# Kernel tuning notes

Measured on AMD Instinct MI355X. Metric: run time of the kernel, lower is better.

The kernel has to match this reference:

```python
import jax, jax.numpy as jnp
import numpy as np

VOCAB_SIZE = 32000
HIDDEN_DIM = 1024
NUM_BUF_ACTIONS = 128
BATCH = 64
SEQ_LEN = 512


def setup_inputs() -> dict:
    key = jax.random.key(0)
    ks = jax.random.split(key, 8)
    H = HIDDEN_DIM
    x = jax.random.randint(ks[0], (BATCH, SEQ_LEN), 0, VOCAB_SIZE, dtype=jnp.int32)
    true_actions = jax.random.randint(ks[1], (BATCH, SEQ_LEN), 0, NUM_BUF_ACTIONS, dtype=jnp.int32)
    true_states = jax.random.randint(ks[2], (BATCH, SEQ_LEN), 0, NUM_BUF_ACTIONS, dtype=jnp.int32)
    use_forcing = 0
    # Learned params: embedding table, LSTM input/recurrent kernels (gate order i,f,g,o), dense head
    embed = jax.random.normal(ks[3], (VOCAB_SIZE, H), dtype=jnp.float32) * 0.02
    Wi = jax.random.normal(ks[4], (H, 4 * H), dtype=jnp.float32) * (1.0 / np.sqrt(H))
    Wh = jax.random.normal(ks[5], (H, 4 * H), dtype=jnp.float32) * (1.0 / np.sqrt(H))
    bh = jnp.zeros((4 * H,), dtype=jnp.float32)
    Wo = jax.random.normal(ks[6], (H, NUM_BUF_ACTIONS), dtype=jnp.float32) * (1.0 / np.sqrt(H))
    bo = jnp.zeros((NUM_BUF_ACTIONS,), dtype=jnp.float32)
    return {"embed": embed, "Wi": Wi, "Wh": Wh, "bh": bh, "Wo": Wo, "bo": bo,
            "x": x, "true_actions": true_actions, "true_states": true_states,
            "use_forcing": use_forcing}


def _lstm_forward(embed, Wi, Wh, bh, Wo, bo, x):
    B, S = x.shape
    H = embed.shape[1]
    x_emb = embed[x]                                    # [B,S,H]
    # Precompute input-side gate projections for all timesteps (one big GEMM)
    gx = jnp.einsum('bsh,hg->sbg', x_emb, Wi)           # [S,B,4H]
    c0 = jnp.zeros((B, H), dtype=x_emb.dtype)
    h0 = jnp.zeros((B, H), dtype=x_emb.dtype)

    def step(carry, gx_t):
        c, h = carry
        gates = gx_t + h @ Wh + bh                      # [B,4H]
        i, f, g, o = jnp.split(gates, 4, axis=-1)
        i = jax.nn.sigmoid(i)
        f = jax.nn.sigmoid(f)
        g = jnp.tanh(g)
        o = jax.nn.sigmoid(o)
        c = f * c + i * g
        h = o * jnp.tanh(c)
        return (c, h), h

    _, hs = jax.lax.scan(step, (c0, h0), gx)            # hs: [S,B,H]
    hs = jnp.transpose(hs, (1, 0, 2))                   # [B,S,H]
    logits_buf = hs @ Wo + bo                           # [B,S,A]
    dummy = jnp.zeros((B, S, 1), dtype=logits_buf.dtype)
    return dummy, logits_buf, dummy


def reference(embed, Wi, Wh, bh, Wo, bo, x, true_actions, true_states, use_forcing):
    # true_actions/true_states/use_forcing are unused in the original forward
    return _lstm_forward(embed, Wi, Wh, bh, Wo, bo, x)
```

## Files before the change

### kernel.cpp

```cpp
#include <hip/hip_runtime.h>
#include <hip/hip_bf16.h>

typedef __attribute__((ext_vector_type(8))) short short8;
typedef __attribute__((ext_vector_type(4))) float float4v;
typedef __attribute__((ext_vector_type(4))) unsigned int uint4v;
typedef unsigned short ushort_t;
typedef unsigned int uint_t;

#define BB 64
#define SS 512
#define HH 1024
#define AA 128
#define NWG 256

#define XSW_BYTES   67108864ULL
#define WSW_BYTES   16777216ULL
#define HALL_BYTES  67239936ULL
#define XSW_OFF     0ULL
#define WSW_OFF     (XSW_OFF + XSW_BYTES)
#define HALL_OFF    (WSW_OFF + WSW_BYTES)
#define FLAGS_OFF   (HALL_OFF + HALL_BYTES)

__device__ __forceinline__ ushort_t f2bf(float f) {
    union { float f; uint_t u; } v; v.f = f;
    uint_t u = v.u;
    return (ushort_t)((u + 0x7fffu + ((u >> 16) & 1u)) >> 16);
}

__device__ __forceinline__ float fast_sigmoid(float x) {
    return __builtin_amdgcn_rcpf(1.0f + __expf(-x));
}
__device__ __forceinline__ float fast_tanh(float x) {
    return 1.0f - 2.0f * __builtin_amdgcn_rcpf(1.0f + __expf(2.0f * x));
}

__global__ void k_init(uint_t* __restrict__ flags, ushort_t* __restrict__ hall,
                       float* __restrict__ out) {
    int i = blockIdx.x * 256 + threadIdx.x;
    if (i < NWG) flags[i] = 0u;
    ((uint_t*)hall)[i] = 0u;
    out[i] = 0.0f;
    out[32768 + (size_t)BB * SS * AA + i] = 0.0f;
}

__global__ void k_prep_x(const float* __restrict__ embed, const int* __restrict__ x,
                         ushort_t* __restrict__ xsw) {
    int t = blockIdx.x * 256 + threadIdx.x;
    int lane = t & 63;
    int rg   = (t >> 6) & 3;
    int kk   = (t >> 8) & 31;
    int s    = t >> 13;
    int b  = rg * 16 + (lane & 15);
    int k0 = kk * 32 + (lane >> 4) * 8;
    int tok = x[b * SS + s];
    const float* src = embed + (size_t)tok * HH + k0;
    float4v v0 = *(const float4v*)src;
    float4v v1 = *(const float4v*)(src + 4);
    uint_t p0 = (uint_t)f2bf(v0[0]) | ((uint_t)f2bf(v0[1]) << 16);
    uint_t p1 = (uint_t)f2bf(v0[2]) | ((uint_t)f2bf(v0[3]) << 16);
    uint_t p2 = (uint_t)f2bf(v1[0]) | ((uint_t)f2bf(v1[1]) << 16);
    uint_t p3 = (uint_t)f2bf(v1[2]) | ((uint_t)f2bf(v1[3]) << 16);
    uint4v pk = {p0, p1, p2, p3};
    ((uint4v*)xsw)[t] = pk;
}

__global__ void k_prep_w(const float* __restrict__ Wi, const float* __restrict__ Wh,
                         ushort_t* __restrict__ wsw) {
    int t = blockIdx.x * 256 + threadIdx.x;
    int u = t & 1023;
    int q = (t >> 10) & 3;
    int k = t >> 12;
    float v = (k < 1024) ? Wi[(size_t)k * 4096 + q * 1024 + u]
                         : Wh[(size_t)(k - 1024) * 4096 + q * 1024 + u];
    int g = u >> 2, du = u & 3;
    int c = du * 4 + q;
    int kk = k >> 5, quad = (k >> 3) & 3, j = k & 7;
    int lane = quad * 16 + c;
    wsw[(((size_t)g * 64 + kk) * 64 + lane) * 8 + j] = f2bf(v);
}

__global__ void __launch_bounds__(256)
k_lstm(const ushort_t* __restrict__ xsw, const ushort_t* __restrict__ wsw,
       ushort_t* hall, const float* __restrict__ bh, uint_t* flags) {
    __shared__ ushort_t wlds[64 * 64 * 8];
    const int g    = blockIdx.x;
    const int tid  = threadIdx.x;
    const int lane = tid & 63;
    const int rg   = tid >> 6;

    {
        const uint4v* src = (const uint4v*)(wsw + (size_t)g * 64 * 64 * 8);
        uint4v* dst = (uint4v*)wlds;
        for (int i = tid; i < 4096; i += 256) dst[i] = src[i];
    }
    __syncthreads();

    const int c_idx = lane & 15;
    const int q  = c_idx & 3;
    const int du = c_idx >> 2;
    const int quad = lane >> 4;
    const int u = g * 4 + du;
    const float bhv = bh[q * 1024 + u];

    const int kk_h = u >> 5;
    const int quad_h = (u & 31) >> 3;
    const int j_h = u & 7;
    uint_t* hall32 = (uint_t*)hall;

    float cst0 = 0.f, cst1 = 0.f, cst2 = 0.f, cst3 = 0.f;
    const short8* xbase = (const short8*)xsw;
    const short8* hbase = (const short8*)hall;
    const short8* wl = (const short8*)wlds + lane;

    for (int s = 0; s < SS; ++s) {
        float4v ac0 = {bhv, bhv, bhv, bhv};
        float4v ac1 = {0.f, 0.f, 0.f, 0.f};
        float4v ac2 = {0.f, 0.f, 0.f, 0.f};
        float4v ac3 = {0.f, 0.f, 0.f, 0.f};

        const short8* xp = xbase + (((size_t)s * 32) * 4 + rg) * 64 + lane;
        #pragma unroll
        for (int kk = 0; kk < 32; kk += 4) {
            short8 a0 = xp[(kk + 0) * 256];
            short8 a1 = xp[(kk + 1) * 256];
            short8 a2 = xp[(kk + 2) * 256];
            short8 a3 = xp[(kk + 3) * 256];
            ac0 = __builtin_amdgcn_mfma_f32_16x16x32_bf16(a0, wl[(kk + 0) * 64], ac0, 0, 0, 0);
            ac1 = __builtin_amdgcn_mfma_f32_16x16x32_bf16(a1, wl[(kk + 1) * 64], ac1, 0, 0, 0);
            ac2 = __builtin_amdgcn_mfma_f32_16x16x32_bf16(a2, wl[(kk + 2) * 64], ac2, 0, 0, 0);
            ac3 = __builtin_amdgcn_mfma_f32_16x16x32_bf16(a3, wl[(kk + 3) * 64], ac3, 0, 0, 0);
        }

        {
            bool ok;
            do {
                uint_t f = __hip_atomic_load(&flags[tid], __ATOMIC_RELAXED,
                                             __HIP_MEMORY_SCOPE_AGENT);
                ok = (f >= (uint_t)s);
            } while (!__syncthreads_and(ok));
            asm volatile("" ::: "memory");
        }

        const short8* hp = hbase + (((size_t)s * 32) * 4 + rg) * 64 + lane;
        #pragma unroll
        for (int kk = 0; kk < 32; kk += 4) {
            short8 a0 = hp[(kk + 0) * 256];
            short8 a1 = hp[(kk + 1) * 256];
            short8 a2 = hp[(kk + 2) * 256];
            short8 a3 = hp[(kk + 3) * 256];
            ac0 = __builtin_amdgcn_mfma_f32_16x16x32_bf16(a0, wl[(32 + kk + 0) * 64], ac0, 0, 0, 0);
            ac1 = __builtin_amdgcn_mfma_f32_16x16x32_bf16(a1, wl[(32 + kk + 1) * 64], ac1, 0, 0, 0);
            ac2 = __builtin_amdgcn_mfma_f32_16x16x32_bf16(a2, wl[(32 + kk + 2) * 64], ac2, 0, 0, 0);
            ac3 = __builtin_amdgcn_mfma_f32_16x16x32_bf16(a3, wl[(32 + kk + 3) * 64], ac3, 0, 0, 0);
        }
        float4v acc = (ac0 + ac1) + (ac2 + ac3);

        float hv[4];
        #pragma unroll
        for (int r = 0; r < 4; ++r) {
            float own = acc[r];
            float a = (q == 2) ? fast_tanh(own) : fast_sigmoid(own);
            float x1 = __shfl_xor(a, 1);
            float x2 = __shfl_xor(a, 2);
            float x3 = __shfl_xor(a, 3);
            float gi, gf, gg, go;
            if      (q == 0) { gi = a;  gf = x1; gg = x2; go = x3; }
            else if (q == 1) { gi = x1; gf = a;  gg = x3; go = x2; }
            else if (q == 2) { gi = x2; gf = x3; gg = a;  go = x1; }
            else             { gi = x3; gf = x2; gg = x1; go = a;  }
            float cv = (r == 0 ? cst0 : r == 1 ? cst1 : r == 2 ? cst2 : cst3);
            cv = gf * cv + gi * gg;
            if (r == 0) cst0 = cv; else if (r == 1) cst1 = cv;
            else if (r == 2) cst2 = cv; else cst3 = cv;
            hv[r] = go * fast_tanh(cv);
        }

        float pv0 = __shfl_xor(hv[0], 4);
        float pv1 = __shfl_xor(hv[1], 4);
        float pv2 = __shfl_xor(hv[2], 4);
        float pv3 = __shfl_xor(hv[3], 4);
        if (q == 0 && (du & 1) == 0) {
            float pv[4] = {pv0, pv1, pv2, pv3};
            size_t base = (((size_t)(s + 1) * 32 + kk_h) * 4 + rg) * 64;
            #pragma unroll
            for (int r = 0; r < 4; ++r) {
                uint_t packed = (uint_t)f2bf(hv[r]) | ((uint_t)f2bf(pv[r]) << 16);
                int lane_h = quad_h * 16 + quad * 4 + r;
                size_t idx = ((base + (size_t)lane_h) * 8 + j_h) >> 1;
                __hip_atomic_store(&hall32[idx], packed, __ATOMIC_RELAXED,
                                   __HIP_MEMORY_SCOPE_AGENT);
            }
        }
        __syncthreads();
        if (tid == 0)
            __hip_atomic_store(&flags[g], (uint_t)(s + 1), __ATOMIC_RELAXED,
                               __HIP_MEMORY_SCOPE_AGENT);
    }
}

__global__ void __launch_bounds__(256)
k_head(const ushort_t* __restrict__ hall, const float* __restrict__ Wo,
       const float* __restrict__ bo, float* __restrict__ out) {
    __shared__ ushort_t wlds[32 * 2 * 64 * 8];
    const int wg = blockIdx.x;
    const int cg = wg & 3, sg = wg >> 2;
    const int tid = threadIdx.x, lane = tid & 63, rg = tid >> 6;
    const int col0 = cg * 32;

    for (int i = tid; i < 32768; i += 256) {
        int k = i >> 5;
        int col = i & 31;
        float v = Wo[(size_t)k * AA + col0 + col];
        int kk = k >> 5, quad = (k >> 3) & 3, j = k & 7;
        int nt = col >> 4, cl = col & 15;
        wlds[(((kk * 2 + nt) * 64) + quad * 16 + cl) * 8 + j] = f2bf(v);
    }
    __syncthreads();

    const int cl = lane & 15, quad = lane >> 4;
    const float bo0 = bo[col0 + cl];
    const float bo1 = bo[col0 + 16 + cl];
    const short8* wl = (const short8*)wlds + lane;

    for (int si = 0; si < 4; ++si) {
        int s = sg * 4 + si;
        float4v a0 = {bo0, bo0, bo0, bo0};
        float4v a1 = {bo1, bo1, bo1, bo1};
        const short8* hp = (const short8*)hall + (((size_t)(s + 1) * 32) * 4 + rg) * 64 + lane;
        #pragma unroll 8
        for (int kk = 0; kk < 32; ++kk) {
            short8 a = hp[kk * 256];
            a0 = __builtin_amdgcn_mfma_f32_16x16x32_bf16(a, wl[(kk * 2 + 0) * 64], a0, 0, 0, 0);
            a1 = __builtin_amdgcn_mfma_f32_16x16x32_bf16(a, wl[(kk * 2 + 1) * 64], a1, 0, 0, 0);
        }
        #pragma unroll
        for (int r = 0; r < 4; ++r) {
            int b = rg * 16 + quad * 4 + r;
            size_t o = 32768 + ((size_t)b * SS + s) * AA;
            out[o + col0 + cl]      = a0[r];
            out[o + col0 + 16 + cl] = a1[r];
        }
    }
}

extern "C" void kernel_launch(void* const* d_in, const int* in_sizes, int n_in,
                              void* d_out, int out_size, void* d_ws, size_t ws_size,
                              hipStream_t stream) {
    const float* embed = (const float*)d_in[0];
    const float* Wi    = (const float*)d_in[1];
    const float* Wh    = (const float*)d_in[2];
    const float* bh    = (const float*)d_in[3];
    const float* Wo    = (const float*)d_in[4];
    const float* bo    = (const float*)d_in[5];
    const int*   x     = (const int*)d_in[6];
    float* out = (float*)d_out;
    unsigned char* ws = (unsigned char*)d_ws;

    ushort_t* xsw  = (ushort_t*)(ws + XSW_OFF);
    ushort_t* wsw  = (ushort_t*)(ws + WSW_OFF);
    ushort_t* hall = (ushort_t*)(ws + HALL_OFF);
    uint_t*   flags = (uint_t*)(ws + FLAGS_OFF);

    k_init  <<<128,   256, 0, stream>>>(flags, hall, out);
    k_prep_x<<<16384, 256, 0, stream>>>(embed, x, xsw);
    k_prep_w<<<32768, 256, 0, stream>>>(Wi, Wh, wsw);
    k_lstm  <<<NWG,   256, 0, stream>>>(xsw, wsw, hall, bh, flags);
    k_head  <<<512,   256, 0, stream>>>(hall, Wo, bo, out);
}
```

Measured before the change: 2.795 ms.

## Merge two LSTM hidden slices per workgroup to halve grid-barrier participants

The persistent LSTM kernel now runs 128 workgroups of 512 threads instead of 256 of 256. Each workgroup keeps two hidden-unit slices of weights in LDS, 128 KB in total, and each group of four waves handles one slice. The per-timestep spin-wait now polls only 128 flags, which is meant to cut cross-workgroup synchronisation latency. In exchange each CU does twice the MFMA and load work per step while half the CUs sit idle, and LDS use doubles.

Result: slower. 5.189 ms (+85.7%).

```diff
diff --git a/kernel.cpp b/kernel.cpp
--- a/kernel.cpp
+++ b/kernel.cpp
@@ -11,7 +11,7 @@
 #define SS 512
 #define HH 1024
 #define AA 128
-#define NWG 256
+#define NWG 128
 
 #define XSW_BYTES   67108864ULL
 #define WSW_BYTES   16777216ULL
@@ -20,6 +20,8 @@
 #define WSW_OFF     (XSW_OFF + XSW_BYTES)
 #define HALL_OFF    (WSW_OFF + WSW_BYTES)
 #define FLAGS_OFF   (HALL_OFF + HALL_BYTES)
+
+#define MFMA __builtin_amdgcn_mfma_f32_16x16x32_bf16
 
 __device__ __forceinline__ ushort_t f2bf(float f) {
     union { float f; uint_t u; } v; v.f = f;
@@ -79,19 +81,21 @@
     wsw[(((size_t)g * 64 + kk) * 64 + lane) * 8 + j] = f2bf(v);
 }
 
-__global__ void __launch_bounds__(256)
+__global__ void __launch_bounds__(512)
 k_lstm(const ushort_t* __restrict__ xsw, const ushort_t* __restrict__ wsw,
        ushort_t* hall, const float* __restrict__ bh, uint_t* flags) {
-    __shared__ ushort_t wlds[64 * 64 * 8];
+    __shared__ ushort_t wlds[2 * 64 * 64 * 8];
     const int g    = blockIdx.x;
     const int tid  = threadIdx.x;
     const int lane = tid & 63;
-    const int rg   = tid >> 6;
+    const int w    = tid >> 6;
+    const int rg   = w & 3;
+    const int tle  = w >> 2;
 
     {
-        const uint4v* src = (const uint4v*)(wsw + (size_t)g * 64 * 64 * 8);
+        const uint4v* src = (const uint4v*)(wsw + (size_t)(2 * g) * 64 * 64 * 8);
         uint4v* dst = (uint4v*)wlds;
-        for (int i = tid; i < 4096; i += 256) dst[i] = src[i];
+        for (int i = tid; i < 8192; i += 512) dst[i] = src[i];
     }
     __syncthreads();
 
@@ -99,18 +103,19 @@
     const int q  = c_idx & 3;
     const int du = c_idx >> 2;
     const int quad = lane >> 4;
-    const int u = g * 4 + du;
+    const int sl = 2 * g + tle;
+    const int u  = sl * 4 + du;
     const float bhv = bh[q * 1024 + u];
 
     const int kk_h = u >> 5;
     const int quad_h = (u & 31) >> 3;
     const int j_h = u & 7;
     uint_t* hall32 = (uint_t*)hall;
-
-    float cst0 = 0.f, cst1 = 0.f, cst2 = 0.f, cst3 = 0.f;
     const short8* xbase = (const short8*)xsw;
     const short8* hbase = (const short8*)hall;
-    const short8* wl = (const short8*)wlds + lane;
+    const short8* wl = (const short8*)wlds + (tle << 12) + lane;
+
+    float cst0 = 0.f, cst1 = 0.f, cst2 = 0.f, cst3 = 0.f;
 
     for (int s = 0; s < SS; ++s) {
         float4v ac0 = {bhv, bhv, bhv, bhv};
@@ -125,16 +130,16 @@
             short8 a1 = xp[(kk + 1) * 256];
             short8 a2 = xp[(kk + 2) * 256];
             short8 a3 = xp[(kk + 3) * 256];
-            ac0 = __builtin_amdgcn_mfma_f32_16x16x32_bf16(a0, wl[(kk + 0) * 64], ac0, 0, 0, 0);
-            ac1 = __builtin_amdgcn_mfma_f32_16x16x32_bf16(a1, wl[(kk + 1) * 64], ac1, 0, 0, 0);
-            ac2 = __builtin_amdgcn_mfma_f32_16x16x32_bf16(a2, wl[(kk + 2) * 64], ac2, 0, 0, 0);
-            ac3 = __builtin_amdgcn_mfma_f32_16x16x32_bf16(a3, wl[(kk + 3) * 64], ac3, 0, 0, 0);
+            ac0 = MFMA(a0, wl[(kk + 0) * 64], ac0, 0, 0, 0);
+            ac1 = MFMA(a1, wl[(kk + 1) * 64], ac1, 0, 0, 0);
+            ac2 = MFMA(a2, wl[(kk + 2) * 64], ac2, 0, 0, 0);
+            ac3 = MFMA(a3, wl[(kk + 3) * 64], ac3, 0, 0, 0);
         }
 
         {
             bool ok;
             do {
-                uint_t f = __hip_atomic_load(&flags[tid], __ATOMIC_RELAXED,
+                uint_t f = __hip_atomic_load(&flags[tid & (NWG - 1)], __ATOMIC_RELAXED,
                                              __HIP_MEMORY_SCOPE_AGENT);
                 ok = (f >= (uint_t)s);
             } while (!__syncthreads_and(ok));
@@ -148,10 +153,10 @@
             short8 a1 = hp[(kk + 1) * 256];
             short8 a2 = hp[(kk + 2) * 256];
             short8 a3 = hp[(kk + 3) * 256];
-            ac0 = __builtin_amdgcn_mfma_f32_16x16x32_bf16(a0, wl[(32 + kk + 0) * 64], ac0, 0, 0, 0);
-            ac1 = __builtin_amdgcn_mfma_f32_16x16x32_bf16(a1, wl[(32 + kk + 1) * 64], ac1, 0, 0, 0);
-            ac2 = __builtin_amdgcn_mfma_f32_16x16x32_bf16(a2, wl[(32 + kk + 2) * 64], ac2, 0, 0, 0);
-            ac3 = __builtin_amdgcn_mfma_f32_16x16x32_bf16(a3, wl[(32 + kk + 3) * 64], ac3, 0, 0, 0);
+            ac0 = MFMA(a0, wl[(32 + kk + 0) * 64], ac0, 0, 0, 0);
+            ac1 = MFMA(a1, wl[(32 + kk + 1) * 64], ac1, 0, 0, 0);
+            ac2 = MFMA(a2, wl[(32 + kk + 2) * 64], ac2, 0, 0, 0);
+            ac3 = MFMA(a3, wl[(32 + kk + 3) * 64], ac3, 0, 0, 0);
         }
         float4v acc = (ac0 + ac1) + (ac2 + ac3);
 
@@ -230,8 +235,8 @@
         #pragma unroll 8
         for (int kk = 0; kk < 32; ++kk) {
             short8 a = hp[kk * 256];
-            a0 = __builtin_amdgcn_mfma_f32_16x16x32_bf16(a, wl[(kk * 2 + 0) * 64], a0, 0, 0, 0);
-            a1 = __builtin_amdgcn_mfma_f32_16x16x32_bf16(a, wl[(kk * 2 + 1) * 64], a1, 0, 0, 0);
+            a0 = MFMA(a, wl[(kk * 2 + 0) * 64], a0, 0, 0, 0);
+            a1 = MFMA(a, wl[(kk * 2 + 1) * 64], a1, 0, 0, 0);
         }
         #pragma unroll
         for (int r = 0; r < 4; ++r) {
@@ -264,6 +269,6 @@
     k_init  <<<128,   256, 0, stream>>>(flags, hall, out);
     k_prep_x<<<16384, 256, 0, stream>>>(embed, x, xsw);
     k_prep_w<<<32768, 256, 0, stream>>>(Wi, Wh, wsw);
-    k_lstm  <<<NWG,   256, 0, stream>>>(xsw, wsw, hall, bh, flags);
+    k_lstm  <<<NWG,   512, 0, stream>>>(xsw, wsw, hall, bh, flags);
     k_head  <<<512,   256, 0, stream>>>(hall, Wo, bo, out);
 }
```
